# Optimization experiments

Hardware: AMD Instinct MI355X
Metric: run time of the kernel (lower is better)

Reference implementation:

```python
import jax, jax.numpy as jnp
import numpy as np

E = 1024      # attSize
R = 2048      # resSize
B = 16384
TOPK = 80
EPS = 1e-12


def _mlp(x, W1, b1, W2, b2):
    # Linear -> ReLU -> Linear (torch Linear: y = x @ W.T + b)
    h = jax.nn.relu(x @ W1.T + b1)
    return h @ W2.T + b2


def _l2norm(x):
    n = jnp.linalg.norm(x, axis=1, keepdims=True)
    return x / jnp.maximum(n, EPS)


def setup_inputs() -> dict:
    key = jax.random.key(0)
    ks = jax.random.split(key, 32)
    s = 0.02
    d = {
        "semantic_global": jax.random.normal(ks[0], (B, E), jnp.float32),
        "semantic_local": jax.random.normal(ks[1], (B, E), jnp.float32),
        "visual_feat": jax.random.normal(ks[2], (B, R), jnp.float32),
    }
    names = ["Wgu1", "Wgu2", "Wgd1", "Wgd2", "Wlu1", "Wlu2", "Wld1", "Wld2", "Wo"]
    for i, n in enumerate(names):
        d[n] = jax.random.normal(ks[3 + i], (E, E), jnp.float32) * s
        d["b" + n[1:]] = jnp.zeros((E,), jnp.float32)
    # MultiheadAttention packed in_proj: [3E, E] (q, k, v stacked)
    d["Win"] = jax.random.normal(ks[20], (3 * E, E), jnp.float32) * s
    d["bin_"] = jnp.zeros((3 * E,), jnp.float32)
    return d


def reference(semantic_global, semantic_local, visual_feat,
              Wgu1, bgu1, Wgu2, bgu2, Wgd1, bgd1, Wgd2, bgd2,
              Wlu1, blu1, Wlu2, blu2, Wld1, bld1, Wld2, bld2,
              Wo, bo, Win, bin_):
    sg = jax.nn.sigmoid(_mlp(semantic_global, Wgu1, bgu1, Wgu2, bgu2)) * \
         _mlp(semantic_global, Wgd1, bgd1, Wgd2, bgd2)
    sl = jax.nn.sigmoid(_mlp(semantic_local, Wlu1, blu1, Wlu2, blu2)) * \
         _mlp(semantic_local, Wld1, bld1, Wld2, bld2)

    # MultiheadAttention with seq_len=1: softmax over a single key is 1,
    # so output = out_proj(v_proj(value)) exactly.
    Wv, bv = Win[2 * E:], bin_[2 * E:]
    def attn_out(value):
        v = value @ Wv.T + bv
        return v @ Wo.T + bo

    fused_feat1 = _l2norm(attn_out(sg))   # self-attn on global
    fused_feat2 = _l2norm(attn_out(sl))   # cross-attn (kv = local)

    final_fused_feat = jax.nn.sigmoid(fused_feat1) * fused_feat2

    # top-k by |value|, keep original signed values, zeros elsewhere
    _, idx = jax.lax.top_k(jnp.abs(final_fused_feat), TOPK)   # [B, 80]
    vals = jnp.take_along_axis(final_fused_feat, idx, axis=1)
    rows = jnp.arange(final_fused_feat.shape[0])[:, None]
    sparse_feat = jnp.zeros_like(final_fused_feat).at[rows, idx].set(vals)

    fused_feat = jnp.concatenate([visual_feat, sparse_feat], axis=1)
    return (fused_feat, final_fused_feat, fused_feat2)
```

## Files before the change

kernel.cpp:

```cpp
#include <hip/hip_runtime.h>

typedef __bf16 bf16_t;
typedef __bf16 bf16x4 __attribute__((ext_vector_type(4)));
typedef __bf16 bf16x8 __attribute__((ext_vector_type(8)));
typedef float f32x4 __attribute__((ext_vector_type(4)));
typedef int i32x4v __attribute__((ext_vector_type(4)));
typedef int i32x8v __attribute__((ext_vector_type(8)));

#define GLL16(gp, lp) __builtin_amdgcn_global_load_lds( \
    (__attribute__((address_space(1))) void*)(gp),      \
    (__attribute__((address_space(3))) void*)(lp), 16, 0, 0)

__device__ inline unsigned char f32_to_fp8(float v)
{
    return (unsigned char)(__builtin_amdgcn_cvt_pk_fp8_f32(v, v, 0, false) & 0xff);
}

__device__ inline i32x8v join8(i32x4v a, i32x4v b)
{
    i32x8v r;
    r[0] = a[0]; r[1] = a[1]; r[2] = a[2]; r[3] = a[3];
    r[4] = b[0]; r[5] = b[1]; r[6] = b[2]; r[7] = b[3];
    return r;
}

template<int EPI>
__global__ __launch_bounds__(256, 4)
void gemm128_f8(const unsigned char* __restrict__ A0,
                const unsigned char* __restrict__ A1, int lda,
                const unsigned char* __restrict__ W0,
                const unsigned char* __restrict__ W1,
                const float* __restrict__ bias0, const float* __restrict__ bias1,
                const unsigned char* __restrict__ U0,
                const unsigned char* __restrict__ U1,
                void* __restrict__ C0v, void* __restrict__ C1v, int ldc,
                int K, int nbx, int nbyH, int ctot)
{
    __shared__ __attribute__((aligned(64))) unsigned char As[128 * 128];
    __shared__ __attribute__((aligned(64))) unsigned char Bs[128 * 128];

    const int t = threadIdx.x;
    const int w = t >> 6, l = t & 63;
    const int wr = w >> 1, wc = w & 1;
    const int ro = l & 15, hi = l >> 4;
    const int sw = ro & 7;
    const int gA = (((hi << 1) ^ sw) * 16);

    const int xcd   = blockIdx.x & 7;
    const int local = blockIdx.x >> 3;
    const int wpb   = ctot >> 2;
    const int win   = local >> 5;
    const int r5    = local & 31;
    const int strp  = win / wpb;
    const int wcn   = win - strp * wpb;
    const int byh   = xcd * (nbyH >> 3) + strp * 8 + (r5 >> 2);
    const int c     = wcn * 4 + (r5 & 3);
    const int sel   = (c >= nbx) ? 1 : 0;
    const int bx    = c - sel * nbx;

    const unsigned char* A    = sel ? A1 : A0;
    const unsigned char* W    = sel ? W1 : W0;
    const float*  bias = sel ? bias1 : bias0;
    const unsigned char* Up = sel ? U1 : U0;
    void*         Cp   = sel ? C1v : C0v;

    const unsigned char* Ab = A + (size_t)byh * 128 * lda;
    const unsigned char* Wb = W + (size_t)bx * 128 * K;

    const int trow = t >> 3;
    const int cg   = (t & 7) ^ (trow & 7);
    const unsigned char* asrc = Ab + (size_t)trow * lda + cg * 16;
    const unsigned char* bsrc = Wb + (size_t)trow * K   + cg * 16;
    int koff = 0;

    f32x4 acc[4][4] = {};

    for (int kt = 0; kt < K; kt += 128) {
#pragma unroll
        for (int r = 0; r < 4; ++r) {
            GLL16(asrc + (size_t)r * 32 * lda + koff, &As[(r * 256 + w * 64) * 16]);
            GLL16(bsrc + (size_t)r * 32 * K   + koff, &Bs[(r * 256 + w * 64) * 16]);
        }
        koff += 128;
        __syncthreads();
        i32x8v bq[4];
#pragma unroll
        for (int n = 0; n < 4; ++n) {
            const unsigned char* bp = Bs + (wc * 64 + n * 16 + ro) * 128;
            bq[n] = join8(*(const i32x4v*)(bp + gA),
                          *(const i32x4v*)(bp + (gA ^ 16)));
        }
#pragma unroll
        for (int m = 0; m < 4; ++m) {
            const unsigned char* ap = As + (wr * 64 + m * 16 + ro) * 128;
            const i32x8v af = join8(*(const i32x4v*)(ap + gA),
                                    *(const i32x4v*)(ap + (gA ^ 16)));
#pragma unroll
            for (int n = 0; n < 4; ++n)
                acc[m][n] = __builtin_amdgcn_mfma_scale_f32_16x16x128_f8f6f4(
                    af, bq[n], acc[m][n], 0, 0,
                    0, 0x7F7F7F7F,
                    0, 0x7B7B7B7B);
        }
        __syncthreads();
    }

    const int rbase = byh * 128 + wr * 64 + (hi << 2);
    const int cbase = bx * 128 + wc * 64 + ro;
    float bc[4];
#pragma unroll
    for (int n = 0; n < 4; ++n) bc[n] = bias[cbase + n * 16];
#pragma unroll
    for (int m = 0; m < 4; ++m) {
#pragma unroll
        for (int j = 0; j < 4; ++j) {
            const int row = rbase + m * 16 + j;
            const size_t off = (size_t)row * ldc + cbase;
            bf16_t* pd = (bf16_t*)Cp + ((row >> 14) ? 1024 : 0)
                       + (size_t)(row & 16383) * 6144 + cbase;
#pragma unroll
            for (int n = 0; n < 4; ++n) {
                float v = acc[m][n][j] + bc[n];
                if (EPI == 0) v = fmaxf(v, 0.0f);
                if (EPI == 2) {
                    const float u = __builtin_amdgcn_cvt_f32_fp8(
                        (int)Up[off + n * 16], 0);
                    v *= 1.0f / (1.0f + __expf(-u));
                }
                if (EPI == 3)      ((float*)Cp)[off + n * 16] = v;
                else if (EPI == 4) pd[n * 16] = (bf16_t)v;
                else ((unsigned char*)Cp)[off + n * 16] = f32_to_fp8(v);
            }
        }
    }
}

__global__ __launch_bounds__(256, 2)
void gemm_small_bt(const bf16_t* __restrict__ A, int lda,
                   const bf16_t* __restrict__ W,
                   unsigned char* __restrict__ C, int ldc, int K)
{
    __shared__ bf16_t As[128 * 64];
    __shared__ bf16_t Bs[128 * 64];
    const int t = threadIdx.x;
    const int w = t >> 6, l = t & 63;
    const int wr = w >> 1, wc = w & 1;

    const bf16_t* Ab = A + (size_t)blockIdx.y * 128 * lda;
    const bf16_t* Wb = W + (size_t)blockIdx.x * 128 * K;

    const bf16_t* asrc[4];
    const bf16_t* bsrc[4];
#pragma unroll
    for (int r = 0; r < 4; ++r) {
        const int seg = r * 256 + t;
        asrc[r] = Ab + (size_t)(seg >> 3) * lda + (seg & 7) * 8;
        bsrc[r] = Wb + (size_t)(seg >> 3) * K   + (seg & 7) * 8;
    }

    f32x4 acc[4][4] = {};

    for (int kt = 0; kt < K; kt += 64) {
#pragma unroll
        for (int r = 0; r < 4; ++r) {
            GLL16(asrc[r], As + (r * 256 + w * 64) * 8);
            GLL16(bsrc[r], Bs + (r * 256 + w * 64) * 8);
            asrc[r] += 64;
            bsrc[r] += 64;
        }
        __syncthreads();
#pragma unroll
        for (int kk = 0; kk < 2; ++kk) {
            const int ro = l & 15;
            const int ko = kk * 32 + (l >> 4) * 8;
            bf16x8 af[4], bqv[4];
#pragma unroll
            for (int m = 0; m < 4; ++m)
                af[m] = *(const bf16x8*)(As + (wr * 64 + m * 16 + ro) * 64 + ko);
#pragma unroll
            for (int n = 0; n < 4; ++n)
                bqv[n] = *(const bf16x8*)(Bs + (wc * 64 + n * 16 + ro) * 64 + ko);
#pragma unroll
            for (int m = 0; m < 4; ++m)
#pragma unroll
                for (int n = 0; n < 4; ++n)
                    acc[m][n] = __builtin_amdgcn_mfma_f32_16x16x32_bf16(
                        af[m], bqv[n], acc[m][n], 0, 0, 0);
        }
        __syncthreads();
    }

    const int rbase = blockIdx.y * 128 + wr * 64 + ((l >> 4) << 2);
    const int cbase = blockIdx.x * 128 + wc * 64 + (l & 15);
#pragma unroll
    for (int m = 0; m < 4; ++m)
#pragma unroll
        for (int j = 0; j < 4; ++j) {
            const int row = rbase + m * 16 + j;
#pragma unroll
            for (int n = 0; n < 4; ++n)
                C[(size_t)row * ldc + cbase + n * 16] =
                    f32_to_fp8(acc[m][n][j] * 16.0f);
        }
}

struct PrepArgs {
    const float* w[8];
    const float* Wo; const float* Wv;
    const float* SG; const float* SL;
    const float* bgu1; const float* bgd1;
    const float* blu1; const float* bld1;
    const float* bv;  const float* bo;
    unsigned char* Wf8; bf16_t* Wo_b; bf16_t* WvT;
    unsigned char* X; unsigned char* Y;
    float* bb; float* bvo;
};

__global__ __launch_bounds__(256)
void prep(PrepArgs a)
{
    __shared__ bf16_t tile[64][65];
    __shared__ float ws4[4];
    int b = blockIdx.x;
    const int t = threadIdx.x;

    if (b < 4096) {
        const int region = b >> 9;
        const float* src = a.w[region];
        const size_t base = (size_t)(b & 511) * 2048 + t * 8;
        const float4 f0 = *(const float4*)(src + base);
        const float4 f1 = *(const float4*)(src + base + 4);
        int x = __builtin_amdgcn_cvt_pk_fp8_f32(f0.x * 16.f, f0.y * 16.f, 0, false);
        x     = __builtin_amdgcn_cvt_pk_fp8_f32(f0.z * 16.f, f0.w * 16.f, x, true);
        int y = __builtin_amdgcn_cvt_pk_fp8_f32(f1.x * 16.f, f1.y * 16.f, 0, false);
        y     = __builtin_amdgcn_cvt_pk_fp8_f32(f1.z * 16.f, f1.w * 16.f, y, true);
        *(int2*)(a.Wf8 + ((size_t)region << 20) + base) = make_int2(x, y);
        return;
    }
    b -= 4096;
    if (b < 16384) {
        const float* src = (b < 8192) ? a.SG : a.SL;
        unsigned char* dst = (b < 8192) ? a.X : a.Y;
        const size_t i = ((size_t)(b & 8191) * 256 + t) * 8;
        const float4 f0 = *(const float4*)(src + i);
        const float4 f1 = *(const float4*)(src + i + 4);
        int x = __builtin_amdgcn_cvt_pk_fp8_f32(f0.x, f0.y, 0, false);
        x     = __builtin_amdgcn_cvt_pk_fp8_f32(f0.z, f0.w, x, true);
        int y = __builtin_amdgcn_cvt_pk_fp8_f32(f1.x, f1.y, 0, false);
        y     = __builtin_amdgcn_cvt_pk_fp8_f32(f1.z, f1.w, y, true);
        *(int2*)(dst + i) = make_int2(x, y);
        return;
    }
    b -= 16384;
    if (b < 1024) {
        const size_t i = ((size_t)b * 256 + t) * 4;
        const float4 f = *(const float4*)(a.Wo + i);
        bf16x4 h = {(bf16_t)f.x, (bf16_t)f.y, (bf16_t)f.z, (bf16_t)f.w};
        *(bf16x4*)(a.Wo_b + i) = h;
        return;
    }
    b -= 1024;
    if (b < 256) {
        const int bm = (b >> 4) * 64, bk = (b & 15) * 64;
#pragma unroll
        for (int s = 0; s < 4; ++s) {
            const int r = s * 16 + (t >> 4);
            const int c = (t & 15) * 4;
            const float4 f = *(const float4*)(a.Wv + (size_t)(bm + r) * 1024 + bk + c);
            tile[r][c] = (bf16_t)f.x; tile[r][c + 1] = (bf16_t)f.y;
            tile[r][c + 2] = (bf16_t)f.z; tile[r][c + 3] = (bf16_t)f.w;
        }
        __syncthreads();
#pragma unroll
        for (int s = 0; s < 4; ++s) {
            const int k = s * 16 + (t >> 4);
            const int m = (t & 15) * 4;
            bf16x4 v = {tile[m][k], tile[m + 1][k], tile[m + 2][k], tile[m + 3][k]};
            *(bf16x4*)(a.WvT + (size_t)(bk + k) * 1024 + bm + m) = v;
        }
        return;
    }
    b -= 256;
    if (b < 16) {
        const float* pa = (b < 8) ? a.bgu1 : a.blu1;
        const float* pb = (b < 8) ? a.bgd1 : a.bld1;
        float* dst = a.bb + ((b < 8) ? 0 : 2048);
        const int i = (b & 7) * 256 + t;
        if (i < 1024) dst[i] = pa[i];
        else dst[i] = pb[i - 1024];
        return;
    }
    b -= 16;
    {
        const float* wr = a.Wo + (size_t)b * 1024;
        float s = 0.0f;
#pragma unroll
        for (int i = 0; i < 4; ++i) s += wr[t + i * 256] * a.bv[t + i * 256];
#pragma unroll
        for (int o = 32; o > 0; o >>= 1) s += __shfl_down(s, o);
        if ((t & 63) == 0) ws4[t >> 6] = s;
        __syncthreads();
        if (t == 0) a.bvo[b] = ws4[0] + ws4[1] + ws4[2] + ws4[3] + a.bo[b];
    }
}

__global__ __launch_bounds__(256)
void finalize_topk(float* __restrict__ OUT2, float* __restrict__ OUT3,
                   const float* __restrict__ VIS, float* __restrict__ O1)
{
    const int row = blockIdx.x, t = threadIdx.x;
    __shared__ int bins[256];
    __shared__ float wred[8];
    __shared__ int wsum[4];
    __shared__ int s_sel, s_kk, s_done;

    float* o1r = O1 + (size_t)row * 3072;
    const bf16_t* prow = (const bf16_t*)o1r;
    float av[4], lv[4];
    {
        const bf16x4 pg = *(const bf16x4*)(prow + t * 4);
        const bf16x4 pl = *(const bf16x4*)(prow + 1024 + t * 4);
#pragma unroll
        for (int j = 0; j < 4; ++j) { av[j] = (float)pg[j]; lv[j] = (float)pl[j]; }
    }
    __syncthreads();

    float sa = 0.0f, sb = 0.0f;
#pragma unroll
    for (int j = 0; j < 4; ++j) { sa += av[j] * av[j]; sb += lv[j] * lv[j]; }
#pragma unroll
    for (int o = 32; o > 0; o >>= 1) {
        sa += __shfl_down(sa, o);
        sb += __shfl_down(sb, o);
    }
    if ((t & 63) == 0) { wred[t >> 6] = sa; wred[4 + (t >> 6)] = sb; }
    __syncthreads();
    const float sca = 1.0f / fmaxf(sqrtf(wred[0] + wred[1] + wred[2] + wred[3]), 1e-12f);
    const float scl = 1.0f / fmaxf(sqrtf(wred[4] + wred[5] + wred[6] + wred[7]), 1e-12f);

    float fv[4], f2v[4];
    unsigned ab[4];
#pragma unroll
    for (int j = 0; j < 4; ++j) {
        const float f2 = lv[j] * scl;
        const float f1 = av[j] * sca;
        const float fin = f2 / (1.0f + __expf(-f1));
        f2v[j] = f2; fv[j] = fin;
        ab[j] = __float_as_uint(fin) & 0x7fffffffu;
    }
    *(float4*)(OUT3 + (size_t)row * 1024 + t * 4) =
        make_float4(f2v[0], f2v[1], f2v[2], f2v[3]);
    *(float4*)(OUT2 + (size_t)row * 1024 + t * 4) =
        make_float4(fv[0], fv[1], fv[2], fv[3]);

    const float* vr = VIS + (size_t)row * 2048;
    *(float4*)(o1r + t * 4)        = *(const float4*)(vr + t * 4);
    *(float4*)(o1r + 1024 + t * 4) = *(const float4*)(vr + 1024 + t * 4);

    unsigned pref = 0u, msk = 0u;
    int kk = 80;
    bool early = false;
    for (int bp = 3; bp >= 0; --bp) {
        bins[t] = 0;
        __syncthreads();
#pragma unroll
        for (int j = 0; j < 4; ++j)
            if ((ab[j] & msk) == pref)
                atomicAdd(&bins[(ab[j] >> (bp * 8)) & 255], 1);
        __syncthreads();
        const int x = bins[t];
        int p = x;
#pragma unroll
        for (int o = 1; o < 64; o <<= 1) {
            const int y = __shfl_up(p, o);
            if ((t & 63) >= o) p += y;
        }
        if ((t & 63) == 63) wsum[t >> 6] = p;
        __syncthreads();
        const int tot = wsum[0] + wsum[1] + wsum[2] + wsum[3];
        int off = 0;
        if ((t >> 6) > 0) off += wsum[0];
        if ((t >> 6) > 1) off += wsum[1];
        if ((t >> 6) > 2) off += wsum[2];
        p += off;
        const int Sme = tot - p + x;
        const int Snx = tot - p;
        if (Sme >= kk && Snx < kk) {
            s_sel = t; s_kk = kk - Snx; s_done = ((kk - Snx) == x) ? 1 : 0;
        }
        __syncthreads();
        pref |= (unsigned)s_sel << (bp * 8);
        msk  |= 0xFFu << (bp * 8);
        kk = s_kk;
        if (s_done) { early = true; break; }
        __syncthreads();
    }

    if (early) {
#pragma unroll
        for (int j = 0; j < 4; ++j) {
            const bool kp = ((ab[j] & msk) >= pref);
            o1r[2048 + t * 4 + j] = kp ? fv[j] : 0.0f;
        }
        return;
    }

    int ec = 0;
#pragma unroll
    for (int j = 0; j < 4; ++j) ec += (ab[j] == pref) ? 1 : 0;
    int pe = ec;
#pragma unroll
    for (int o = 1; o < 64; o <<= 1) {
        const int y = __shfl_up(pe, o);
        if ((t & 63) >= o) pe += y;
    }
    if ((t & 63) == 63) wsum[t >> 6] = pe;
    __syncthreads();
    int off2 = 0;
    if ((t >> 6) > 0) off2 += wsum[0];
    if ((t >> 6) > 1) off2 += wsum[1];
    if ((t >> 6) > 2) off2 += wsum[2];
    int excl = pe + off2 - ec;
#pragma unroll
    for (int j = 0; j < 4; ++j) {
        const bool eq = (ab[j] == pref);
        const bool kp = (ab[j] > pref) || (eq && (excl < kk));
        o1r[2048 + t * 4 + j] = kp ? fv[j] : 0.0f;
        if (eq) ++excl;
    }
}

extern "C" void kernel_launch(void* const* d_in, const int* in_sizes, int n_in,
                              void* d_out, int out_size, void* d_ws, size_t ws_size,
                              hipStream_t stream)
{
    const float* SG   = (const float*)d_in[0];
    const float* SL   = (const float*)d_in[1];
    const float* VIS  = (const float*)d_in[2];
    const float* Wgu1 = (const float*)d_in[3];
    const float* bgu1 = (const float*)d_in[4];
    const float* Wgu2 = (const float*)d_in[5];  const float* bgu2 = (const float*)d_in[6];
    const float* Wgd1 = (const float*)d_in[7];  const float* bgd1 = (const float*)d_in[8];
    const float* Wgd2 = (const float*)d_in[9];  const float* bgd2 = (const float*)d_in[10];
    const float* Wlu1 = (const float*)d_in[11]; const float* blu1 = (const float*)d_in[12];
    const float* Wlu2 = (const float*)d_in[13]; const float* blu2 = (const float*)d_in[14];
    const float* Wld1 = (const float*)d_in[15]; const float* bld1 = (const float*)d_in[16];
    const float* Wld2 = (const float*)d_in[17]; const float* bld2 = (const float*)d_in[18];
    const float* Wo   = (const float*)d_in[19]; const float* bo   = (const float*)d_in[20];
    const float* Win  = (const float*)d_in[21]; const float* bin_ = (const float*)d_in[22];
    const float* Wv = Win + (size_t)2 * 1024 * 1024;
    const float* bv = bin_ + 2048;

    float* OUT1 = (float*)d_out;
    float* OUT2 = OUT1 + (size_t)16384 * 3072;
    float* OUT3 = OUT2 + (size_t)16384 * 1024;

    char* ws = (char*)d_ws;
    unsigned char* Wf8 = (unsigned char*)ws;
    bf16_t* Wo_b = (bf16_t*)(ws + (8u << 20));
    unsigned char* Wvo = (unsigned char*)(ws + (10u << 20));
    float* bb  = (float*)(ws + (11u << 20));
    float* bvo = bb + 4096;

    unsigned char* Ug = (unsigned char*)d_out + (64u << 20);
    unsigned char* Ul = (unsigned char*)d_out + (96u << 20);
    unsigned char* H1g = (unsigned char*)d_out + (128u << 20);
    unsigned char* H1l = H1g + (32u << 20);
    bf16_t* WvT = (bf16_t*)H1g;
    unsigned char* X = (unsigned char*)d_out + (192u << 20);
    unsigned char* Y = X + (16u << 20);

    PrepArgs pa;
    pa.w[0] = Wgu1; pa.w[1] = Wgd1; pa.w[2] = Wlu1; pa.w[3] = Wld1;
    pa.w[4] = Wgu2; pa.w[5] = Wgd2; pa.w[6] = Wlu2; pa.w[7] = Wld2;
    pa.Wo = Wo; pa.Wv = Wv; pa.SG = SG; pa.SL = SL;
    pa.bgu1 = bgu1; pa.bgd1 = bgd1; pa.blu1 = blu1; pa.bld1 = bld1;
    pa.bv = bv; pa.bo = bo;
    pa.Wf8 = Wf8; pa.Wo_b = Wo_b; pa.WvT = WvT;
    pa.X = X; pa.Y = Y; pa.bb = bb; pa.bvo = bvo;

    prep<<<22800, 256, 0, stream>>>(pa);

    gemm_small_bt<<<dim3(8, 8), 256, 0, stream>>>(Wo_b, 1024, WvT, Wvo, 1024, 1024);

    unsigned char* Wg1   = Wf8;
    unsigned char* Wl1   = Wf8 + (size_t)2 * 1048576;
    unsigned char* Wgu2b = Wf8 + (size_t)4 * 1048576;
    unsigned char* Wgd2b = Wf8 + (size_t)5 * 1048576;
    unsigned char* Wlu2b = Wf8 + (size_t)6 * 1048576;
    unsigned char* Wld2b = Wf8 + (size_t)7 * 1048576;

    gemm128_f8<0><<<4096, 256, 0, stream>>>(X, Y, 1024, Wg1, Wl1, bb, bb + 2048,
                                            nullptr, nullptr, H1g, H1l, 2048, 1024, 16, 128, 32);
    gemm128_f8<1><<<2048, 256, 0, stream>>>(H1g, H1l, 2048, Wgu2b, Wlu2b, bgu2, blu2,
                                            nullptr, nullptr, Ug, Ul, 1024, 1024, 8, 128, 16);
    gemm128_f8<2><<<2048, 256, 0, stream>>>(H1g + 1024, H1l + 1024, 2048, Wgd2b, Wld2b,
                                            bgd2, bld2, Ug, Ul, X, Y, 1024, 1024, 8, 128, 16);
    gemm128_f8<4><<<2048, 256, 0, stream>>>(X, X, 1024, Wvo, Wvo, bvo, bvo,
                                            nullptr, nullptr, OUT1, OUT1, 6144, 1024, 8, 256, 8);

    finalize_topk<<<16384, 256, 0, stream>>>(OUT2, OUT3, VIS, OUT1);
}
```

Baseline: 380.6 us.

## Fuse Wo·Wv weight product GEMM into prep kernel and use nontemporal memory ops

The separate bf16 conversion of Wo, the transpose of Wv and the small GEMM kernel that formed the combined Wvo weight are replaced by 64 extra blocks inside the prep kernel. These blocks load fp32 Wo/Wv directly, convert to bf16 in LDS and run the MFMA product, which removes one kernel launch and the intermediate bf16 buffers. Streaming loads and stores in prep and finalize_topk are switched to nontemporal builtins to reduce cache pollution. The in-prep GEMM reads B with scalar strided LDS accesses, which may cause bank conflicts, and its larger LDS footprint applies to every prep block and can lower occupancy for the conversion blocks.

After: 350.7 us. -7.9%, faster.

```diff
diff --git a/kernel.cpp b/kernel.cpp
--- a/kernel.cpp
+++ b/kernel.cpp
@@ -135,75 +135,6 @@
     }
 }
 
-__global__ __launch_bounds__(256, 2)
-void gemm_small_bt(const bf16_t* __restrict__ A, int lda,
-                   const bf16_t* __restrict__ W,
-                   unsigned char* __restrict__ C, int ldc, int K)
-{
-    __shared__ bf16_t As[128 * 64];
-    __shared__ bf16_t Bs[128 * 64];
-    const int t = threadIdx.x;
-    const int w = t >> 6, l = t & 63;
-    const int wr = w >> 1, wc = w & 1;
-
-    const bf16_t* Ab = A + (size_t)blockIdx.y * 128 * lda;
-    const bf16_t* Wb = W + (size_t)blockIdx.x * 128 * K;
-
-    const bf16_t* asrc[4];
-    const bf16_t* bsrc[4];
-#pragma unroll
-    for (int r = 0; r < 4; ++r) {
-        const int seg = r * 256 + t;
-        asrc[r] = Ab + (size_t)(seg >> 3) * lda + (seg & 7) * 8;
-        bsrc[r] = Wb + (size_t)(seg >> 3) * K   + (seg & 7) * 8;
-    }
-
-    f32x4 acc[4][4] = {};
-
-    for (int kt = 0; kt < K; kt += 64) {
-#pragma unroll
-        for (int r = 0; r < 4; ++r) {
-            GLL16(asrc[r], As + (r * 256 + w * 64) * 8);
-            GLL16(bsrc[r], Bs + (r * 256 + w * 64) * 8);
-            asrc[r] += 64;
-            bsrc[r] += 64;
-        }
-        __syncthreads();
-#pragma unroll
-        for (int kk = 0; kk < 2; ++kk) {
-            const int ro = l & 15;
-            const int ko = kk * 32 + (l >> 4) * 8;
-            bf16x8 af[4], bqv[4];
-#pragma unroll
-            for (int m = 0; m < 4; ++m)
-                af[m] = *(const bf16x8*)(As + (wr * 64 + m * 16 + ro) * 64 + ko);
-#pragma unroll
-            for (int n = 0; n < 4; ++n)
-                bqv[n] = *(const bf16x8*)(Bs + (wc * 64 + n * 16 + ro) * 64 + ko);
-#pragma unroll
-            for (int m = 0; m < 4; ++m)
-#pragma unroll
-                for (int n = 0; n < 4; ++n)
-                    acc[m][n] = __builtin_amdgcn_mfma_f32_16x16x32_bf16(
-                        af[m], bqv[n], acc[m][n], 0, 0, 0);
-        }
-        __syncthreads();
-    }
-
-    const int rbase = blockIdx.y * 128 + wr * 64 + ((l >> 4) << 2);
-    const int cbase = blockIdx.x * 128 + wc * 64 + (l & 15);
-#pragma unroll
-    for (int m = 0; m < 4; ++m)
-#pragma unroll
-        for (int j = 0; j < 4; ++j) {
-            const int row = rbase + m * 16 + j;
-#pragma unroll
-            for (int n = 0; n < 4; ++n)
-                C[(size_t)row * ldc + cbase + n * 16] =
-                    f32_to_fp8(acc[m][n][j] * 16.0f);
-        }
-}
-
 struct PrepArgs {
     const float* w[8];
     const float* Wo; const float* Wv;
@@ -211,7 +142,7 @@
     const float* bgu1; const float* bgd1;
     const float* blu1; const float* bld1;
     const float* bv;  const float* bo;
-    unsigned char* Wf8; bf16_t* Wo_b; bf16_t* WvT;
+    unsigned char* Wf8; unsigned char* Wvo;
     unsigned char* X; unsigned char* Y;
     float* bb; float* bvo;
 };
@@ -219,21 +150,85 @@
 __global__ __launch_bounds__(256)
 void prep(PrepArgs a)
 {
-    __shared__ bf16_t tile[64][65];
+    __shared__ bf16_t AsC[128 * 72];
+    __shared__ bf16_t BsC[64 * 128];
     __shared__ float ws4[4];
     int b = blockIdx.x;
     const int t = threadIdx.x;
 
+    if (b < 64) {
+        const int by = b >> 3, bx = b & 7;
+        const int n0 = by * 128, k0 = bx * 128;
+        const int w = t >> 6, l = t & 63;
+        const int wr = w >> 1, wc = w & 1;
+        const int ro = l & 15, hi = l >> 4;
+        f32x4 acc[4][4] = {};
+        for (int mt = 0; mt < 1024; mt += 64) {
+#pragma unroll
+            for (int r = 0; r < 8; ++r) {
+                const int row = r * 16 + (t >> 4);
+                const int col = (t & 15) * 4;
+                const f32x4 f = *(const f32x4*)(a.Wo + (size_t)(n0 + row) * 1024 + mt + col);
+                bf16x4 h = {(bf16_t)f[0], (bf16_t)f[1], (bf16_t)f[2], (bf16_t)f[3]};
+                *(bf16x4*)(AsC + row * 72 + col) = h;
+            }
+#pragma unroll
+            for (int r = 0; r < 8; ++r) {
+                const int mr = r * 8 + (t >> 5);
+                const int kc = (t & 31) * 4;
+                const f32x4 f = *(const f32x4*)(a.Wv + (size_t)(mt + mr) * 1024 + k0 + kc);
+                bf16x4 h = {(bf16_t)f[0], (bf16_t)f[1], (bf16_t)f[2], (bf16_t)f[3]};
+                *(bf16x4*)(BsC + mr * 128 + kc) = h;
+            }
+            __syncthreads();
+#pragma unroll
+            for (int kk = 0; kk < 2; ++kk) {
+                const int ko = kk * 32 + hi * 8;
+                bf16x8 af[4], bq[4];
+#pragma unroll
+                for (int m = 0; m < 4; ++m)
+                    af[m] = *(const bf16x8*)(AsC + (wr * 64 + m * 16 + ro) * 72 + ko);
+#pragma unroll
+                for (int n = 0; n < 4; ++n) {
+                    const int j = wc * 64 + n * 16 + ro;
+#pragma unroll
+                    for (int e = 0; e < 8; ++e)
+                        bq[n][e] = BsC[(ko + e) * 128 + j];
+                }
+#pragma unroll
+                for (int m = 0; m < 4; ++m)
+#pragma unroll
+                    for (int n = 0; n < 4; ++n)
+                        acc[m][n] = __builtin_amdgcn_mfma_f32_16x16x32_bf16(
+                            af[m], bq[n], acc[m][n], 0, 0, 0);
+            }
+            __syncthreads();
+        }
+        const int rbase = n0 + wr * 64 + (hi << 2);
+        const int cbase = k0 + wc * 64 + ro;
+#pragma unroll
+        for (int m = 0; m < 4; ++m)
+#pragma unroll
+            for (int j = 0; j < 4; ++j) {
+                const int row = rbase + m * 16 + j;
+#pragma unroll
+                for (int n = 0; n < 4; ++n)
+                    a.Wvo[(size_t)row * 1024 + cbase + n * 16] =
+                        f32_to_fp8(acc[m][n][j] * 16.0f);
+            }
+        return;
+    }
+    b -= 64;
     if (b < 4096) {
         const int region = b >> 9;
         const float* src = a.w[region];
         const size_t base = (size_t)(b & 511) * 2048 + t * 8;
-        const float4 f0 = *(const float4*)(src + base);
-        const float4 f1 = *(const float4*)(src + base + 4);
-        int x = __builtin_amdgcn_cvt_pk_fp8_f32(f0.x * 16.f, f0.y * 16.f, 0, false);
-        x     = __builtin_amdgcn_cvt_pk_fp8_f32(f0.z * 16.f, f0.w * 16.f, x, true);
-        int y = __builtin_amdgcn_cvt_pk_fp8_f32(f1.x * 16.f, f1.y * 16.f, 0, false);
-        y     = __builtin_amdgcn_cvt_pk_fp8_f32(f1.z * 16.f, f1.w * 16.f, y, true);
+        const f32x4 f0 = __builtin_nontemporal_load((const f32x4*)(src + base));
+        const f32x4 f1 = __builtin_nontemporal_load((const f32x4*)(src + base + 4));
+        int x = __builtin_amdgcn_cvt_pk_fp8_f32(f0[0] * 16.f, f0[1] * 16.f, 0, false);
+        x     = __builtin_amdgcn_cvt_pk_fp8_f32(f0[2] * 16.f, f0[3] * 16.f, x, true);
+        int y = __builtin_amdgcn_cvt_pk_fp8_f32(f1[0] * 16.f, f1[1] * 16.f, 0, false);
+        y     = __builtin_amdgcn_cvt_pk_fp8_f32(f1[2] * 16.f, f1[3] * 16.f, y, true);
         *(int2*)(a.Wf8 + ((size_t)region << 20) + base) = make_int2(x, y);
         return;
     }
@@ -242,45 +237,16 @@
         const float* src = (b < 8192) ? a.SG : a.SL;
         unsigned char* dst = (b < 8192) ? a.X : a.Y;
         const size_t i = ((size_t)(b & 8191) * 256 + t) * 8;
-        const float4 f0 = *(const float4*)(src + i);
-        const float4 f1 = *(const float4*)(src + i + 4);
-        int x = __builtin_amdgcn_cvt_pk_fp8_f32(f0.x, f0.y, 0, false);
-        x     = __builtin_amdgcn_cvt_pk_fp8_f32(f0.z, f0.w, x, true);
-        int y = __builtin_amdgcn_cvt_pk_fp8_f32(f1.x, f1.y, 0, false);
-        y     = __builtin_amdgcn_cvt_pk_fp8_f32(f1.z, f1.w, y, true);
+        const f32x4 f0 = __builtin_nontemporal_load((const f32x4*)(src + i));
+        const f32x4 f1 = __builtin_nontemporal_load((const f32x4*)(src + i + 4));
+        int x = __builtin_amdgcn_cvt_pk_fp8_f32(f0[0], f0[1], 0, false);
+        x     = __builtin_amdgcn_cvt_pk_fp8_f32(f0[2], f0[3], x, true);
+        int y = __builtin_amdgcn_cvt_pk_fp8_f32(f1[0], f1[1], 0, false);
+        y     = __builtin_amdgcn_cvt_pk_fp8_f32(f1[2], f1[3], y, true);
         *(int2*)(dst + i) = make_int2(x, y);
         return;
     }
     b -= 16384;
-    if (b < 1024) {
-        const size_t i = ((size_t)b * 256 + t) * 4;
-        const float4 f = *(const float4*)(a.Wo + i);
-        bf16x4 h = {(bf16_t)f.x, (bf16_t)f.y, (bf16_t)f.z, (bf16_t)f.w};
-        *(bf16x4*)(a.Wo_b + i) = h;
-        return;
-    }
-    b -= 1024;
-    if (b < 256) {
-        const int bm = (b >> 4) * 64, bk = (b & 15) * 64;
-#pragma unroll
-        for (int s = 0; s < 4; ++s) {
-            const int r = s * 16 + (t >> 4);
-            const int c = (t & 15) * 4;
-            const float4 f = *(const float4*)(a.Wv + (size_t)(bm + r) * 1024 + bk + c);
-            tile[r][c] = (bf16_t)f.x; tile[r][c + 1] = (bf16_t)f.y;
-            tile[r][c + 2] = (bf16_t)f.z; tile[r][c + 3] = (bf16_t)f.w;
-        }
-        __syncthreads();
-#pragma unroll
-        for (int s = 0; s < 4; ++s) {
-            const int k = s * 16 + (t >> 4);
-            const int m = (t & 15) * 4;
-            bf16x4 v = {tile[m][k], tile[m + 1][k], tile[m + 2][k], tile[m + 3][k]};
-            *(bf16x4*)(a.WvT + (size_t)(bk + k) * 1024 + bm + m) = v;
-        }
-        return;
-    }
-    b -= 256;
     if (b < 16) {
         const float* pa = (b < 8) ? a.bgu1 : a.blu1;
         const float* pb = (b < 8) ? a.bgd1 : a.bld1;
@@ -348,14 +314,20 @@
         f2v[j] = f2; fv[j] = fin;
         ab[j] = __float_as_uint(fin) & 0x7fffffffu;
     }
-    *(float4*)(OUT3 + (size_t)row * 1024 + t * 4) =
-        make_float4(f2v[0], f2v[1], f2v[2], f2v[3]);
-    *(float4*)(OUT2 + (size_t)row * 1024 + t * 4) =
-        make_float4(fv[0], fv[1], fv[2], fv[3]);
+    {
+        f32x4 v2 = {fv[0], fv[1], fv[2], fv[3]};
+        f32x4 v3 = {f2v[0], f2v[1], f2v[2], f2v[3]};
+        __builtin_nontemporal_store(v2, (f32x4*)(OUT2 + (size_t)row * 1024 + t * 4));
+        __builtin_nontemporal_store(v3, (f32x4*)(OUT3 + (size_t)row * 1024 + t * 4));
+    }
 
     const float* vr = VIS + (size_t)row * 2048;
-    *(float4*)(o1r + t * 4)        = *(const float4*)(vr + t * 4);
-    *(float4*)(o1r + 1024 + t * 4) = *(const float4*)(vr + 1024 + t * 4);
+    {
+        const f32x4 a0 = __builtin_nontemporal_load((const f32x4*)(vr + t * 4));
+        const f32x4 a1 = __builtin_nontemporal_load((const f32x4*)(vr + 1024 + t * 4));
+        __builtin_nontemporal_store(a0, (f32x4*)(o1r + t * 4));
+        __builtin_nontemporal_store(a1, (f32x4*)(o1r + 1024 + t * 4));
+    }
 
     unsigned pref = 0u, msk = 0u;
     int kk = 80;
@@ -400,7 +372,7 @@
 #pragma unroll
         for (int j = 0; j < 4; ++j) {
             const bool kp = ((ab[j] & msk) >= pref);
-            o1r[2048 + t * 4 + j] = kp ? fv[j] : 0.0f;
+            __builtin_nontemporal_store(kp ? fv[j] : 0.0f, o1r + 2048 + t * 4 + j);
         }
         return;
     }
@@ -425,7 +397,7 @@
     for (int j = 0; j < 4; ++j) {
         const bool eq = (ab[j] == pref);
         const bool kp = (ab[j] > pref) || (eq && (excl < kk));
-        o1r[2048 + t * 4 + j] = kp ? fv[j] : 0.0f;
+        __builtin_nontemporal_store(kp ? fv[j] : 0.0f, o1r + 2048 + t * 4 + j);
         if (eq) ++excl;
     }
 }
@@ -457,16 +429,14 @@
 
     char* ws = (char*)d_ws;
     unsigned char* Wf8 = (unsigned char*)ws;
-    bf16_t* Wo_b = (bf16_t*)(ws + (8u << 20));
-    unsigned char* Wvo = (unsigned char*)(ws + (10u << 20));
-    float* bb  = (float*)(ws + (11u << 20));
+    unsigned char* Wvo = (unsigned char*)(ws + (8u << 20));
+    float* bb  = (float*)(ws + (9u << 20));
     float* bvo = bb + 4096;
 
     unsigned char* Ug = (unsigned char*)d_out + (64u << 20);
     unsigned char* Ul = (unsigned char*)d_out + (96u << 20);
     unsigned char* H1g = (unsigned char*)d_out + (128u << 20);
     unsigned char* H1l = H1g + (32u << 20);
-    bf16_t* WvT = (bf16_t*)H1g;
     unsigned char* X = (unsigned char*)d_out + (192u << 20);
     unsigned char* Y = X + (16u << 20);
 
@@ -476,12 +446,10 @@
     pa.Wo = Wo; pa.Wv = Wv; pa.SG = SG; pa.SL = SL;
     pa.bgu1 = bgu1; pa.bgd1 = bgd1; pa.blu1 = blu1; pa.bld1 = bld1;
     pa.bv = bv; pa.bo = bo;
-    pa.Wf8 = Wf8; pa.Wo_b = Wo_b; pa.WvT = WvT;
+    pa.Wf8 = Wf8; pa.Wvo = Wvo;
     pa.X = X; pa.Y = Y; pa.bb = bb; pa.bvo = bvo;
 
-    prep<<<22800, 256, 0, stream>>>(pa);
-
-    gemm_small_bt<<<dim3(8, 8), 256, 0, stream>>>(Wo_b, 1024, WvT, Wvo, 1024, 1024);
+    prep<<<21584, 256, 0, stream>>>(pa);
 
     unsigned char* Wg1   = Wf8;
     unsigned char* Wl1   = Wf8 + (size_t)2 * 1048576;
```
